# Kernel tuning notes

Measured on AMD Instinct MI355X. Metric: run time of the kernel, lower is better.

Reference implementation:

```python
import jax, jax.numpy as jnp
import numpy as np

B, N, C = 4, 2048, 1024
H = 8
D = C // H  # head dim = 128
SCALE = D ** -0.5
EPS = 1e-5


def setup_inputs() -> dict:
    key = jax.random.key(0)
    ks = jax.random.split(key, 12)
    s = 0.02
    return {
        "x": jax.random.normal(ks[0], (B, N, C), jnp.float32),
        "ln1_g": jnp.ones((C,), jnp.float32),
        "ln1_b": jnp.zeros((C,), jnp.float32),
        "w_qkv": jax.random.normal(ks[1], (3 * C, C), jnp.float32) * s,  # torch Linear weight [out,in], no bias
        "w_proj": jax.random.normal(ks[2], (C, C), jnp.float32) * s,
        "b_proj": jnp.zeros((C,), jnp.float32),
        "ln2_g": jnp.ones((C,), jnp.float32),
        "ln2_b": jnp.zeros((C,), jnp.float32),
        "w1": jax.random.normal(ks[3], (C, C), jnp.float32) * s,
        "b1": jnp.full((C,), 0.1, jnp.float32),
        "w2": jax.random.normal(ks[4], (C, C), jnp.float32) * s,
        "b2": jnp.full((C,), 0.1, jnp.float32),
        "bn_g": jnp.ones((C,), jnp.float32),
        "bn_b": jnp.zeros((C,), jnp.float32),
        "bn_mean": jnp.zeros((C,), jnp.float32),
        "bn_var": jnp.ones((C,), jnp.float32),
    }


def _layernorm(x, g, b):
    mu = jnp.mean(x, axis=-1, keepdims=True)
    var = jnp.mean(jnp.square(x - mu), axis=-1, keepdims=True)
    return (x - mu) * jax.lax.rsqrt(var + EPS) * g + b


def reference(x, ln1_g, ln1_b, w_qkv, w_proj, b_proj, ln2_g, ln2_b,
              w1, b1, w2, b2, bn_g, bn_b, bn_mean, bn_var):
    # --- attention branch (pre-LN) ---
    h = _layernorm(x, ln1_g, ln1_b)
    qkv = h @ w_qkv.T                              # [B,N,3C]
    qkv = qkv.reshape(B, N, 3, H, D)
    q = qkv[:, :, 0].transpose(0, 2, 1, 3)         # [B,H,N,D]
    k = qkv[:, :, 1].transpose(0, 2, 1, 3)
    v = qkv[:, :, 2].transpose(0, 2, 1, 3)
    attn = jnp.einsum('bhnd,bhmd->bhnm', q, k) * SCALE
    attn = jax.nn.softmax(attn, axis=-1)
    o = jnp.einsum('bhnm,bhmd->bhnd', attn, v)     # [B,H,N,D]
    o = o.transpose(0, 2, 1, 3).reshape(B, N, C)
    x = x + (o @ w_proj.T + b_proj)

    # --- MLP branch (pre-LN), ELU + eval-mode BatchNorm ---
    h = _layernorm(x, ln2_g, ln2_b)
    h = jax.nn.elu(h @ w1.T + b1)
    h = jax.nn.elu(h @ w2.T + b2)
    h = (h - bn_mean) * jax.lax.rsqrt(bn_var + EPS) * bn_g + bn_b
    return x + h
```

## Files before the change

kernel.cpp:

```cpp
#include <hip/hip_runtime.h>
#include <hip/hip_bf16.h>

using u16 = unsigned short;
typedef __attribute__((ext_vector_type(8))) __bf16 bf16x8;
typedef __attribute__((ext_vector_type(4))) float f32x4;
typedef __attribute__((ext_vector_type(16))) float f32x16;
typedef __attribute__((ext_vector_type(4))) unsigned int u32x4;

#define LN_EPS 1e-5f
#define ATT_SCALE 0.08838834764831845f

__device__ __forceinline__ u16 f2bf(float f) {
    unsigned int u = __builtin_bit_cast(unsigned int, f);
    u += 0x7FFFu + ((u >> 16) & 1u);
    return (u16)(u >> 16);
}

__device__ __forceinline__ bf16x8 ld_frag(const u16* p) {
    return __builtin_bit_cast(bf16x8, *(const u32x4*)p);
}

__device__ __forceinline__ unsigned pack_bf2(float lo, float hi) {
    return __builtin_amdgcn_perm(__builtin_bit_cast(unsigned, hi),
                                 __builtin_bit_cast(unsigned, lo), 0x07060302u);
}

__device__ __forceinline__ void gl_lds(const u16* g, u16* l) {
    __builtin_amdgcn_global_load_lds((const __attribute__((address_space(1))) void*)g,
                                     (__attribute__((address_space(3))) void*)l, 16, 0, 0);
}

__global__ __launch_bounds__(256)
void cvt_ln(const float* __restrict__ x, const float* __restrict__ g,
            const float* __restrict__ b, u16* __restrict__ hout,
            const float* __restrict__ w_qkv, const float* __restrict__ w_proj,
            const float* __restrict__ w1, const float* __restrict__ w2,
            u16* __restrict__ wout)
{
    const int t = threadIdx.x;
    if (blockIdx.x < 8192) {
        const int row = blockIdx.x;
        const float4 v = ((const float4*)(x + (size_t)row * 1024))[t];
        float s  = v.x + v.y + v.z + v.w;
        float ss = v.x * v.x + v.y * v.y + v.z * v.z + v.w * v.w;
        #pragma unroll
        for (int d = 32; d > 0; d >>= 1) { s += __shfl_down(s, d); ss += __shfl_down(ss, d); }
        __shared__ float red[8];
        const int wave = t >> 6, lane = t & 63;
        if (lane == 0) { red[wave] = s; red[4 + wave] = ss; }
        __syncthreads();
        const float S  = red[0] + red[1] + red[2] + red[3];
        const float SS = red[4] + red[5] + red[6] + red[7];
        const float mu = S * (1.f / 1024.f);
        const float rstd = rsqrtf(SS * (1.f / 1024.f) - mu * mu + LN_EPS);
        const float4 gv = ((const float4*)g)[t];
        const float4 bv = ((const float4*)b)[t];
        ushort4 ov;
        ov.x = f2bf((v.x - mu) * rstd * gv.x + bv.x);
        ov.y = f2bf((v.y - mu) * rstd * gv.y + bv.y);
        ov.z = f2bf((v.z - mu) * rstd * gv.z + bv.z);
        ov.w = f2bf((v.w - mu) * rstd * gv.w + bv.w);
        ((ushort4*)(hout + (size_t)row * 1024))[t] = ov;
    } else {
        const int i = (blockIdx.x - 8192) * 256 + t;
        const int n_qkv = 3072 * 1024 / 4, n_c = 1024 * 1024 / 4;
        const float* src;
        int j = i;
        if (j < n_qkv) { src = w_qkv; }
        else if ((j -= n_qkv) < n_c) { src = w_proj; }
        else if ((j -= n_c) < n_c)   { src = w1; }
        else { j -= n_c; src = w2; }
        const float4 v = ((const float4*)src)[j];
        ushort4 o;
        o.x = f2bf(v.x); o.y = f2bf(v.y); o.z = f2bf(v.z); o.w = f2bf(v.w);
        ((ushort4*)wout)[i] = o;
    }
}

__global__ __launch_bounds__(256)
void ln_kernel(const float* __restrict__ x, const float* __restrict__ g,
               const float* __restrict__ b, u16* __restrict__ out)
{
    const int row = blockIdx.x;
    const int t = threadIdx.x;
    const float4 v = ((const float4*)(x + (size_t)row * 1024))[t];
    float s  = v.x + v.y + v.z + v.w;
    float ss = v.x * v.x + v.y * v.y + v.z * v.z + v.w * v.w;
    #pragma unroll
    for (int d = 32; d > 0; d >>= 1) { s += __shfl_down(s, d); ss += __shfl_down(ss, d); }
    __shared__ float red[8];
    const int wave = t >> 6, lane = t & 63;
    if (lane == 0) { red[wave] = s; red[4 + wave] = ss; }
    __syncthreads();
    const float S  = red[0] + red[1] + red[2] + red[3];
    const float SS = red[4] + red[5] + red[6] + red[7];
    const float mu = S * (1.f / 1024.f);
    const float rstd = rsqrtf(SS * (1.f / 1024.f) - mu * mu + LN_EPS);
    const float4 gv = ((const float4*)g)[t];
    const float4 bv = ((const float4*)b)[t];
    ushort4 ov;
    ov.x = f2bf((v.x - mu) * rstd * gv.x + bv.x);
    ov.y = f2bf((v.y - mu) * rstd * gv.y + bv.y);
    ov.z = f2bf((v.z - mu) * rstd * gv.z + bv.z);
    ov.w = f2bf((v.w - mu) * rstd * gv.w + bv.w);
    ((ushort4*)(out + (size_t)row * 1024))[t] = ov;
}

__global__ __launch_bounds__(256, 3)
void gemm_qkv(const u16* __restrict__ A, const u16* __restrict__ Bw,
              u16* __restrict__ Cb, u16* __restrict__ Cv)
{
    const int K = 1024;
    __shared__ __align__(16) u16 As[128 * 32];
    __shared__ __align__(16) u16 Bs[128 * 32];

    const int tid  = threadIdx.x;
    const int wave = tid >> 6;
    const int lane = tid & 63;
    const int quad = lane >> 4;
    const int l16  = lane & 15;
    const int m0 = blockIdx.x * 128;
    const int n0 = blockIdx.y * 128;
    const int wm = (wave & 1) * 64;
    const int wn = (wave >> 1) * 64;

    f32x4 acc[4][4];
    #pragma unroll
    for (int i = 0; i < 4; i++)
        #pragma unroll
        for (int j = 0; j < 4; j++)
            acc[i][j] = f32x4{0.f, 0.f, 0.f, 0.f};

    const int srow = lane >> 2;
    const int scol = (lane & 3) * 8;
    const u16* gA0 = A  + (size_t)(m0 + wave * 32 + srow) * K + scol;
    const u16* gA1 = gA0 + (size_t)16 * K;
    const u16* gB0 = Bw + (size_t)(n0 + wave * 32 + srow) * K + scol;
    const u16* gB1 = gB0 + (size_t)16 * K;
    u16* lA0 = &As[(wave * 32) * 32];
    u16* lA1 = &As[(wave * 32 + 16) * 32];
    u16* lB0 = &Bs[(wave * 32) * 32];
    u16* lB1 = &Bs[(wave * 32 + 16) * 32];

    for (int k0 = 0; k0 < K; k0 += 32) {
        gl_lds(gA0 + k0, lA0);
        gl_lds(gA1 + k0, lA1);
        gl_lds(gB0 + k0, lB0);
        gl_lds(gB1 + k0, lB1);
        __syncthreads();
        bf16x8 af[4], bfv[4];
        #pragma unroll
        for (int i = 0; i < 4; i++) af[i]  = ld_frag(&As[(wm + i * 16 + l16) * 32 + quad * 8]);
        #pragma unroll
        for (int j = 0; j < 4; j++) bfv[j] = ld_frag(&Bs[(wn + j * 16 + l16) * 32 + quad * 8]);
        #pragma unroll
        for (int i = 0; i < 4; i++)
            #pragma unroll
            for (int j = 0; j < 4; j++)
                acc[i][j] = __builtin_amdgcn_mfma_f32_16x16x32_bf16(af[i], bfv[j], acc[i][j], 0, 0, 0);
        __syncthreads();
    }

    #pragma unroll
    for (int j = 0; j < 4; j++) {
        const int gn = n0 + wn + j * 16 + l16;
        if (gn < 2048) {
            const float qs = (gn < 1024) ? ATT_SCALE : 1.0f;
            #pragma unroll
            for (int i = 0; i < 4; i++) {
                const int gm0 = m0 + wm + i * 16 + quad * 4;
                #pragma unroll
                for (int r = 0; r < 4; r++)
                    Cb[(size_t)(gm0 + r) * 2048 + gn] = f2bf(acc[i][j][r] * qs);
            }
        } else {
            const int hh = (gn >> 7) & 7, dd = gn & 127;
            #pragma unroll
            for (int i = 0; i < 4; i++) {
                const int gm0 = m0 + wm + i * 16 + quad * 4;
                #pragma unroll
                for (int r = 0; r < 4; r++) {
                    const int tok = gm0 + r;
                    Cv[((size_t)((tok >> 11) * 8 + hh) * 128 + dd) * 2048 + (tok & 2047)] =
                        f2bf(acc[i][j][r]);
                }
            }
        }
    }
}

template <int EPI>
__global__ __launch_bounds__(256, 3)
void gemm_c(const u16* __restrict__ A, const u16* __restrict__ Bw,
            const float* __restrict__ bias, const float* __restrict__ res,
            float* __restrict__ Cf, u16* __restrict__ Cb,
            const float* __restrict__ bng, const float* __restrict__ bnb,
            const float* __restrict__ bnm, const float* __restrict__ bnv)
{
    const int N = 1024, K = 1024;
    __shared__ __align__(16) u16 As[128 * 32];
    __shared__ __align__(16) u16 Bs[128 * 32];

    const int tid  = threadIdx.x;
    const int wave = tid >> 6;
    const int lane = tid & 63;
    const int quad = lane >> 4;
    const int l16  = lane & 15;
    const int m0 = blockIdx.x * 128;
    const int n0 = blockIdx.y * 128;
    const int wm = (wave & 1) * 64;
    const int wn = (wave >> 1) * 64;

    f32x4 acc[4][4];
    #pragma unroll
    for (int i = 0; i < 4; i++)
        #pragma unroll
        for (int j = 0; j < 4; j++)
            acc[i][j] = f32x4{0.f, 0.f, 0.f, 0.f};

    const int srow = lane >> 2;
    const int scol = (lane & 3) * 8;
    const u16* gA0 = A  + (size_t)(m0 + wave * 32 + srow) * K + scol;
    const u16* gA1 = gA0 + (size_t)16 * K;
    const u16* gB0 = Bw + (size_t)(n0 + wave * 32 + srow) * K + scol;
    const u16* gB1 = gB0 + (size_t)16 * K;
    u16* lA0 = &As[(wave * 32) * 32];
    u16* lA1 = &As[(wave * 32 + 16) * 32];
    u16* lB0 = &Bs[(wave * 32) * 32];
    u16* lB1 = &Bs[(wave * 32 + 16) * 32];

    for (int k0 = 0; k0 < K; k0 += 32) {
        gl_lds(gA0 + k0, lA0);
        gl_lds(gA1 + k0, lA1);
        gl_lds(gB0 + k0, lB0);
        gl_lds(gB1 + k0, lB1);
        __syncthreads();
        bf16x8 af[4], bfv[4];
        #pragma unroll
        for (int i = 0; i < 4; i++) af[i]  = ld_frag(&As[(wm + i * 16 + l16) * 32 + quad * 8]);
        #pragma unroll
        for (int j = 0; j < 4; j++) bfv[j] = ld_frag(&Bs[(wn + j * 16 + l16) * 32 + quad * 8]);
        #pragma unroll
        for (int i = 0; i < 4; i++)
            #pragma unroll
            for (int j = 0; j < 4; j++)
                acc[i][j] = __builtin_amdgcn_mfma_f32_16x16x32_bf16(af[i], bfv[j], acc[i][j], 0, 0, 0);
        __syncthreads();
    }

    #pragma unroll
    for (int j = 0; j < 4; j++) {
        const int gn = n0 + wn + j * 16 + l16;
        float bs = bias[gn], sc = 0.f, sh = 0.f;
        if constexpr (EPI == 3) {
            const float iv = rsqrtf(bnv[gn] + LN_EPS);
            sc = bng[gn] * iv;
            sh = bnb[gn] - bnm[gn] * sc;
        }
        #pragma unroll
        for (int i = 0; i < 4; i++) {
            const int gm0 = m0 + wm + i * 16 + quad * 4;
            #pragma unroll
            for (int r = 0; r < 4; r++) {
                const size_t idx = (size_t)(gm0 + r) * N + gn;
                const float v = acc[i][j][r];
                if constexpr (EPI == 1) {
                    Cf[idx] = res[idx] + v + bs;
                } else if constexpr (EPI == 2) {
                    float t = v + bs;
                    t = t > 0.f ? t : (__expf(t) - 1.f);
                    Cb[idx] = f2bf(t);
                } else {
                    float t = v + bs;
                    t = t > 0.f ? t : (__expf(t) - 1.f);
                    t = t * sc + sh;
                    Cf[idx] = res[idx] + t;
                }
            }
        }
    }
}

__global__ __launch_bounds__(256, 2)
void attn_kernel(const u16* __restrict__ qk, const u16* __restrict__ vT, u16* __restrict__ o)
{
    __shared__ __align__(16) u16 smem[32768];

    const int tid  = threadIdx.x;
    const int wave = tid >> 6;
    const int lane = tid & 63;
    const int l32  = lane & 31;
    const int hl   = lane >> 5;
    const int id   = blockIdx.x;
    const int bh   = ((id >> 7) << 3) | (id & 7);
    const int qt   = (id >> 3) & 15;
    const int b    = bh >> 3, h = bh & 7;
    const size_t tok0 = (size_t)b * 2048;

    const u16* qptr = qk + h * 128;
    const u16* kptr = qk + 1024 + h * 128;
    const u16* vptr = vT + (size_t)bh * 128 * 2048;

    #pragma unroll
    for (int qq = 0; qq < 8; qq++) {
        const int s = qq * 256 + tid;
        const int r = s >> 4;
        const int cg = (s & 15) ^ (r & 7);
        const u16* g = qptr + (tok0 + qt * 128 + r) * 2048 + cg * 8;
        const int sb = 16384 + (qq * 256 + (tid & 192)) * 8;
        gl_lds(g, smem + sb);
    }
    __syncthreads();

    bf16x8 qf[8];
    {
        const int row = wave * 32 + l32;
        #pragma unroll
        for (int ks = 0; ks < 8; ks++) {
            const int c = (ks * 2 + hl) ^ (row & 7);
            qf[ks] = ld_frag(smem + 16384 + row * 128 + c * 8);
        }
    }

    f32x16 oacc[4];
    #pragma unroll
    for (int i = 0; i < 4; i++)
        #pragma unroll
        for (int e = 0; e < 16; e++) oacc[i][e] = 0.f;
    float l_acc = 0.f;

    {
        #pragma unroll
        for (int qq = 0; qq < 4; qq++) {
            const int s = qq * 256 + tid;
            const int rk = s >> 4, ck = (s & 15) ^ (rk & 7);
            gl_lds(kptr + (tok0 + rk) * 2048 + ck * 8,
                   smem + (qq * 256 + (tid & 192)) * 8);
            const int rv = s >> 3, cv = (s & 7) ^ (rv & 7);
            gl_lds(vptr + (size_t)rv * 2048 + cv * 8,
                   smem + 8192 + (qq * 256 + (tid & 192)) * 8);
        }
    }

    for (int kt = 0; kt < 32; kt++) {
        __syncthreads();

        if (kt + 1 < 32) {
            u16* nb = smem + ((kt + 1) & 1) * 16384;
            #pragma unroll
            for (int qq = 0; qq < 4; qq++) {
                const int s = qq * 256 + tid;
                const int rk = s >> 4, ck = (s & 15) ^ (rk & 7);
                gl_lds(kptr + (tok0 + (kt + 1) * 64 + rk) * 2048 + ck * 8,
                       nb + (qq * 256 + (tid & 192)) * 8);
                const int rv = s >> 3, cv = (s & 7) ^ (rv & 7);
                gl_lds(vptr + (size_t)rv * 2048 + (kt + 1) * 64 + cv * 8,
                       nb + 8192 + (qq * 256 + (tid & 192)) * 8);
            }
        }

        const u16* Ks = smem + (kt & 1) * 16384;
        const u16* Vs = Ks + 8192;

        f32x16 sacc[2];
        #pragma unroll
        for (int t = 0; t < 2; t++)
            #pragma unroll
            for (int e = 0; e < 16; e++) sacc[t][e] = 0.f;
        __builtin_amdgcn_s_setprio(1);
        #pragma unroll
        for (int ks = 0; ks < 8; ks++) {
            #pragma unroll
            for (int mt = 0; mt < 2; mt++) {
                const int row = mt * 32 + l32;
                const int c = (ks * 2 + hl) ^ (row & 7);
                const bf16x8 kf = ld_frag(Ks + row * 128 + c * 8);
                sacc[mt] = __builtin_amdgcn_mfma_f32_32x32x16_bf16(kf, qf[ks], sacc[mt], 0, 0, 0);
            }
        }
        __builtin_amdgcn_s_setprio(0);

        unsigned pk[2][8];
        #pragma unroll
        for (int t = 0; t < 2; t++) {
            #pragma unroll
            for (int r2 = 0; r2 < 8; r2++) {
                const float p0 = __expf(sacc[t][2 * r2]);
                const float p1 = __expf(sacc[t][2 * r2 + 1]);
                l_acc += p0 + p1;
                pk[t][r2] = pack_bf2(p0, p1);
            }
        }

        #pragma unroll
        for (int ks = 0; ks < 4; ks++) {
            const int t = ks >> 1;
            const int pb = (ks & 1) * 4;
            const unsigned s0 = (unsigned)__shfl_xor((int)pk[t][pb + 0], 32);
            const unsigned s1 = (unsigned)__shfl_xor((int)pk[t][pb + 1], 32);
            const unsigned s2 = (unsigned)__shfl_xor((int)pk[t][pb + 2], 32);
            const unsigned s3 = (unsigned)__shfl_xor((int)pk[t][pb + 3], 32);
            u32x4 pu;
            pu.x = hl ? s2 : pk[t][pb + 0];
            pu.y = hl ? s3 : pk[t][pb + 1];
            pu.z = hl ? pk[t][pb + 2] : s0;
            pu.w = hl ? pk[t][pb + 3] : s1;
            const bf16x8 pf = __builtin_bit_cast(bf16x8, pu);
            __builtin_amdgcn_s_setprio(1);
            #pragma unroll
            for (int dt = 0; dt < 4; dt++) {
                const int row = dt * 32 + l32;
                const int c = (ks * 2 + hl) ^ (row & 7);
                const bf16x8 vf = ld_frag(Vs + row * 64 + c * 8);
                oacc[dt] = __builtin_amdgcn_mfma_f32_32x32x16_bf16(vf, pf, oacc[dt], 0, 0, 0);
            }
            __builtin_amdgcn_s_setprio(0);
        }
    }

    __syncthreads();
    u16* Ot = smem;
    const float lt  = l_acc + __shfl_xor(l_acc, 32);
    const float inv = 1.0f / lt;
    const int qloc = wave * 32 + l32;
    #pragma unroll
    for (int dt = 0; dt < 4; dt++) {
        #pragma unroll
        for (int r2 = 0; r2 < 8; r2++) {
            const float v0 = oacc[dt][2 * r2] * inv;
            const float v1 = oacc[dt][2 * r2 + 1] * inv;
            const int dp = dt * 32 + 4 * hl + 2 * (r2 & 1) + 8 * (r2 >> 1);
            *(unsigned*)(Ot + qloc * 136 + dp) = pack_bf2(v0, v1);
        }
    }
    __syncthreads();
    const int qr = tid >> 1;
    const int hh = tid & 1;
    const u16* src = Ot + qr * 136 + hh * 64;
    u16* dst = o + (tok0 + qt * 128 + qr) * 1024 + h * 128 + hh * 64;
    #pragma unroll
    for (int c = 0; c < 8; c++)
        *(u32x4*)(dst + c * 8) = *(const u32x4*)(src + c * 8);
}

extern "C" void kernel_launch(void* const* d_in, const int* in_sizes, int n_in,
                              void* d_out, int out_size, void* d_ws, size_t ws_size,
                              hipStream_t stream)
{
    const float* x      = (const float*)d_in[0];
    const float* ln1_g  = (const float*)d_in[1];
    const float* ln1_b  = (const float*)d_in[2];
    const float* w_qkv  = (const float*)d_in[3];
    const float* w_proj = (const float*)d_in[4];
    const float* b_proj = (const float*)d_in[5];
    const float* ln2_g  = (const float*)d_in[6];
    const float* ln2_b  = (const float*)d_in[7];
    const float* w1     = (const float*)d_in[8];
    const float* b1     = (const float*)d_in[9];
    const float* w2     = (const float*)d_in[10];
    const float* b2     = (const float*)d_in[11];
    const float* bn_g   = (const float*)d_in[12];
    const float* bn_b   = (const float*)d_in[13];
    const float* bn_m   = (const float*)d_in[14];
    const float* bn_v   = (const float*)d_in[15];
    float* out = (float*)d_out;

    u16* wq   = (u16*)d_ws;
    u16* wp   = wq  + (size_t)3072 * 1024;
    u16* w1b  = wp  + (size_t)1024 * 1024;
    u16* w2b  = w1b + (size_t)1024 * 1024;
    u16* hbuf = w2b + (size_t)1024 * 1024;
    u16* qkb  = hbuf + (size_t)8192 * 1024;
    u16* vTb  = qkb + (size_t)8192 * 2048;
    u16* obuf = vTb + (size_t)8192 * 1024;
    float* x1 = (float*)(obuf + (size_t)8192 * 1024);

    cvt_ln<<<14336, 256, 0, stream>>>(x, ln1_g, ln1_b, hbuf, w_qkv, w_proj, w1, w2, wq);

    gemm_qkv<<<dim3(64, 24), 256, 0, stream>>>(hbuf, wq, qkb, vTb);

    attn_kernel<<<512, 256, 0, stream>>>(qkb, vTb, obuf);

    gemm_c<1><<<dim3(64, 8), 256, 0, stream>>>(obuf, wp,
        b_proj, x, x1, nullptr, nullptr, nullptr, nullptr, nullptr);

    ln_kernel<<<8192, 256, 0, stream>>>(x1, ln2_g, ln2_b, hbuf);

    gemm_c<2><<<dim3(64, 8), 256, 0, stream>>>(hbuf, w1b,
        b1, nullptr, nullptr, obuf, nullptr, nullptr, nullptr, nullptr);

    gemm_c<3><<<dim3(64, 8), 256, 0, stream>>>(obuf, w2b,
        b2, x1, out, nullptr, bn_g, bn_b, bn_m, bn_v);
}
```

Before: 386.5 us.

## Widen GEMM K-tile to 64 with XOR-swizzled LDS and use permlane32_swap in attention

The shared GEMM main loop now stages a 64-wide K slice per iteration into an XOR-swizzled LDS layout, halving the number of barrier pairs and avoiding bank conflicts on fragment reads. The attention P-fragment exchange replaces four cross-half shuffles plus selects with two permlane32_swap instructions. The GEMM change doubles LDS per block, which may lower occupancy, and the swap semantics must match the previous lane mapping.

```diff
diff --git a/kernel.cpp b/kernel.cpp
--- a/kernel.cpp
+++ b/kernel.cpp
@@ -6,6 +6,7 @@
 typedef __attribute__((ext_vector_type(4))) float f32x4;
 typedef __attribute__((ext_vector_type(16))) float f32x16;
 typedef __attribute__((ext_vector_type(4))) unsigned int u32x4;
+typedef __attribute__((ext_vector_type(2))) unsigned int u32x2;
 
 #define LN_EPS 1e-5f
 #define ATT_SCALE 0.08838834764831845f
@@ -106,60 +107,68 @@
     ((ushort4*)(out + (size_t)row * 1024))[t] = ov;
 }
 
+
+#define GEMM_PREAMBLE(Aptr, Bptr, Kdim)                                           \
+    __shared__ __align__(16) u16 As[128 * 64];                                    \
+    __shared__ __align__(16) u16 Bs[128 * 64];                                    \
+    const int tid  = threadIdx.x;                                                 \
+    const int wave = tid >> 6;                                                    \
+    const int lane = tid & 63;                                                    \
+    const int quad = lane >> 4;                                                   \
+    const int l16  = lane & 15;                                                   \
+    const int m0 = blockIdx.x * 128;                                              \
+    const int n0 = blockIdx.y * 128;                                              \
+    const int wm = (wave & 1) * 64;                                               \
+    const int wn = (wave >> 1) * 64;                                              \
+    f32x4 acc[4][4];                                                              \
+    _Pragma("unroll")                                                             \
+    for (int i = 0; i < 4; i++)                                                   \
+        _Pragma("unroll")                                                         \
+        for (int j = 0; j < 4; j++)                                               \
+            acc[i][j] = f32x4{0.f, 0.f, 0.f, 0.f};                                \
+    const int srow8 = lane >> 3;                  \
+    const int scol  = ((lane & 7) ^ srow8) * 8;    \
+    const u16* gA = Aptr + (size_t)(m0 + wave * 8 + srow8) * Kdim + scol;         \
+    const u16* gB = Bptr + (size_t)(n0 + wave * 8 + srow8) * Kdim + scol;         \
+    u16* lA = &As[wave * 512];                                                    \
+    u16* lB = &Bs[wave * 512];                                                    \
+    for (int k0 = 0; k0 < Kdim; k0 += 64) {                                       \
+        _Pragma("unroll")                                                         \
+        for (int rnd = 0; rnd < 4; rnd++) {                                       \
+            gl_lds(gA + (size_t)rnd * 32 * Kdim + k0, lA + rnd * 2048);           \
+            gl_lds(gB + (size_t)rnd * 32 * Kdim + k0, lB + rnd * 2048);           \
+        }                                                                         \
+        __syncthreads();                                                          \
+        _Pragma("unroll")                                                         \
+        for (int kk = 0; kk < 2; kk++) {                                          \
+            bf16x8 af[4], bfv[4];                                                 \
+            _Pragma("unroll")                                                     \
+            for (int i = 0; i < 4; i++) {                                         \
+                const int row = wm + i * 16 + l16;                                \
+                const int c = (kk * 4 + quad) ^ (row & 7);                        \
+                af[i] = ld_frag(&As[row * 64 + c * 8]);                           \
+            }                                                                     \
+            _Pragma("unroll")                                                     \
+            for (int j = 0; j < 4; j++) {                                         \
+                const int row = wn + j * 16 + l16;                                \
+                const int c = (kk * 4 + quad) ^ (row & 7);                        \
+                bfv[j] = ld_frag(&Bs[row * 64 + c * 8]);                          \
+            }                                                                     \
+            _Pragma("unroll")                                                     \
+            for (int i = 0; i < 4; i++)                                           \
+                _Pragma("unroll")                                                 \
+                for (int j = 0; j < 4; j++)                                       \
+                    acc[i][j] = __builtin_amdgcn_mfma_f32_16x16x32_bf16(          \
+                        af[i], bfv[j], acc[i][j], 0, 0, 0);                       \
+        }                                                                         \
+        __syncthreads();                                                          \
+    }
+
 __global__ __launch_bounds__(256, 3)
 void gemm_qkv(const u16* __restrict__ A, const u16* __restrict__ Bw,
               u16* __restrict__ Cb, u16* __restrict__ Cv)
 {
-    const int K = 1024;
-    __shared__ __align__(16) u16 As[128 * 32];
-    __shared__ __align__(16) u16 Bs[128 * 32];
-
-    const int tid  = threadIdx.x;
-    const int wave = tid >> 6;
-    const int lane = tid & 63;
-    const int quad = lane >> 4;
-    const int l16  = lane & 15;
-    const int m0 = blockIdx.x * 128;
-    const int n0 = blockIdx.y * 128;
-    const int wm = (wave & 1) * 64;
-    const int wn = (wave >> 1) * 64;
-
-    f32x4 acc[4][4];
-    #pragma unroll
-    for (int i = 0; i < 4; i++)
-        #pragma unroll
-        for (int j = 0; j < 4; j++)
-            acc[i][j] = f32x4{0.f, 0.f, 0.f, 0.f};
-
-    const int srow = lane >> 2;
-    const int scol = (lane & 3) * 8;
-    const u16* gA0 = A  + (size_t)(m0 + wave * 32 + srow) * K + scol;
-    const u16* gA1 = gA0 + (size_t)16 * K;
-    const u16* gB0 = Bw + (size_t)(n0 + wave * 32 + srow) * K + scol;
-    const u16* gB1 = gB0 + (size_t)16 * K;
-    u16* lA0 = &As[(wave * 32) * 32];
-    u16* lA1 = &As[(wave * 32 + 16) * 32];
-    u16* lB0 = &Bs[(wave * 32) * 32];
-    u16* lB1 = &Bs[(wave * 32 + 16) * 32];
-
-    for (int k0 = 0; k0 < K; k0 += 32) {
-        gl_lds(gA0 + k0, lA0);
-        gl_lds(gA1 + k0, lA1);
-        gl_lds(gB0 + k0, lB0);
-        gl_lds(gB1 + k0, lB1);
-        __syncthreads();
-        bf16x8 af[4], bfv[4];
-        #pragma unroll
-        for (int i = 0; i < 4; i++) af[i]  = ld_frag(&As[(wm + i * 16 + l16) * 32 + quad * 8]);
-        #pragma unroll
-        for (int j = 0; j < 4; j++) bfv[j] = ld_frag(&Bs[(wn + j * 16 + l16) * 32 + quad * 8]);
-        #pragma unroll
-        for (int i = 0; i < 4; i++)
-            #pragma unroll
-            for (int j = 0; j < 4; j++)
-                acc[i][j] = __builtin_amdgcn_mfma_f32_16x16x32_bf16(af[i], bfv[j], acc[i][j], 0, 0, 0);
-        __syncthreads();
-    }
+    GEMM_PREAMBLE(A, Bw, 1024)
 
     #pragma unroll
     for (int j = 0; j < 4; j++) {
@@ -197,56 +206,8 @@
             const float* __restrict__ bng, const float* __restrict__ bnb,
             const float* __restrict__ bnm, const float* __restrict__ bnv)
 {
-    const int N = 1024, K = 1024;
-    __shared__ __align__(16) u16 As[128 * 32];
-    __shared__ __align__(16) u16 Bs[128 * 32];
-
-    const int tid  = threadIdx.x;
-    const int wave = tid >> 6;
-    const int lane = tid & 63;
-    const int quad = lane >> 4;
-    const int l16  = lane & 15;
-    const int m0 = blockIdx.x * 128;
-    const int n0 = blockIdx.y * 128;
-    const int wm = (wave & 1) * 64;
-    const int wn = (wave >> 1) * 64;
-
-    f32x4 acc[4][4];
-    #pragma unroll
-    for (int i = 0; i < 4; i++)
-        #pragma unroll
-        for (int j = 0; j < 4; j++)
-            acc[i][j] = f32x4{0.f, 0.f, 0.f, 0.f};
-
-    const int srow = lane >> 2;
-    const int scol = (lane & 3) * 8;
-    const u16* gA0 = A  + (size_t)(m0 + wave * 32 + srow) * K + scol;
-    const u16* gA1 = gA0 + (size_t)16 * K;
-    const u16* gB0 = Bw + (size_t)(n0 + wave * 32 + srow) * K + scol;
-    const u16* gB1 = gB0 + (size_t)16 * K;
-    u16* lA0 = &As[(wave * 32) * 32];
-    u16* lA1 = &As[(wave * 32 + 16) * 32];
-    u16* lB0 = &Bs[(wave * 32) * 32];
-    u16* lB1 = &Bs[(wave * 32 + 16) * 32];
-
-    for (int k0 = 0; k0 < K; k0 += 32) {
-        gl_lds(gA0 + k0, lA0);
-        gl_lds(gA1 + k0, lA1);
-        gl_lds(gB0 + k0, lB0);
-        gl_lds(gB1 + k0, lB1);
-        __syncthreads();
-        bf16x8 af[4], bfv[4];
-        #pragma unroll
-        for (int i = 0; i < 4; i++) af[i]  = ld_frag(&As[(wm + i * 16 + l16) * 32 + quad * 8]);
-        #pragma unroll
-        for (int j = 0; j < 4; j++) bfv[j] = ld_frag(&Bs[(wn + j * 16 + l16) * 32 + quad * 8]);
-        #pragma unroll
-        for (int i = 0; i < 4; i++)
-            #pragma unroll
-            for (int j = 0; j < 4; j++)
-                acc[i][j] = __builtin_amdgcn_mfma_f32_16x16x32_bf16(af[i], bfv[j], acc[i][j], 0, 0, 0);
-        __syncthreads();
-    }
+    const int N = 1024;
+    GEMM_PREAMBLE(A, Bw, 1024)
 
     #pragma unroll
     for (int j = 0; j < 4; j++) {
@@ -396,15 +357,10 @@
         for (int ks = 0; ks < 4; ks++) {
             const int t = ks >> 1;
             const int pb = (ks & 1) * 4;
-            const unsigned s0 = (unsigned)__shfl_xor((int)pk[t][pb + 0], 32);
-            const unsigned s1 = (unsigned)__shfl_xor((int)pk[t][pb + 1], 32);
-            const unsigned s2 = (unsigned)__shfl_xor((int)pk[t][pb + 2], 32);
-            const unsigned s3 = (unsigned)__shfl_xor((int)pk[t][pb + 3], 32);
+            const u32x2 r02 = __builtin_amdgcn_permlane32_swap(pk[t][pb + 0], pk[t][pb + 2], false, false);
+            const u32x2 r13 = __builtin_amdgcn_permlane32_swap(pk[t][pb + 1], pk[t][pb + 3], false, false);
             u32x4 pu;
-            pu.x = hl ? s2 : pk[t][pb + 0];
-            pu.y = hl ? s3 : pk[t][pb + 1];
-            pu.z = hl ? pk[t][pb + 2] : s0;
-            pu.w = hl ? pk[t][pb + 3] : s1;
+            pu.x = r02.x; pu.y = r13.x; pu.z = r02.y; pu.w = r13.y;
             const bf16x8 pf = __builtin_bit_cast(bf16x8, pu);
             __builtin_amdgcn_s_setprio(1);
             #pragma unroll
```

Measured after the change: 361.8 us. -6.4%, faster.
